# Kernel tuning notes

Hardware: AMD Instinct MI355X
Metric: run time of the kernel (lower is better)

Reference implementation:

```python
import jax, jax.numpy as jnp
import numpy as np

TOP_K_FREQ = 16


def setup_inputs() -> dict:
    key = jax.random.key(0)
    x = jax.random.normal(key, (64, 4096, 128), dtype=jnp.float32)
    return {"x": x}


def reference(x):
    B, L, C = x.shape
    freq = jnp.fft.rfft(x, axis=1)              # [B, F, C] complex, F = L//2 + 1
    F = freq.shape[1]
    k = min(TOP_K_FREQ, F)
    mag = jnp.abs(freq)                          # [B, F, C]
    # top-k over frequency axis, vectorized across (B, C)
    mag_bcf = jnp.transpose(mag, (0, 2, 1))      # [B, C, F]
    _, idx = jax.lax.top_k(mag_bcf, k)           # idx: [B, C, k]
    b_ix = jnp.arange(B)[:, None, None]
    c_ix = jnp.arange(C)[None, :, None]
    mask_bcf = jnp.zeros((B, C, F), dtype=x.dtype).at[b_ix, c_ix, idx].set(1.0)
    mask = jnp.transpose(mask_bcf, (0, 2, 1))    # [B, F, C]
    freq_filtered = freq * mask
    out = jnp.fft.irfft(freq_filtered, n=L, axis=1)  # [B, L, C]
    return out.astype(x.dtype)
```

## Files before the change

kernel.cpp:

```cpp
#include <hip/hip_runtime.h>


#define SWZ(i) ((i) ^ (((i) >> 4) & 15))

__device__ __forceinline__ int drev16(int x) {
  return ((x & 15) << 8) | (x & 0xF0) | ((x >> 8) & 15);
}

__device__ __forceinline__ float2 cmulf(float2 a, float c, float s) {
  return make_float2(a.x * c - a.y * s, a.x * s + a.y * c);
}

__device__ __forceinline__ void bfly4(float2& a0, float2& a1, float2& a2, float2& a3) {
  float ar = a0.x + a2.x, ai = a0.y + a2.y;
  float br = a0.x - a2.x, bi = a0.y - a2.y;
  float cr = a1.x + a3.x, ci = a1.y + a3.y;
  float dr = a1.x - a3.x, di = a1.y - a3.y;
  a0 = make_float2(ar + cr, ai + ci);
  a1 = make_float2(br + di, bi - dr);
  a2 = make_float2(ar - cr, ai - ci);
  a3 = make_float2(br - di, bi + dr);
}

__device__ __forceinline__ void dft16(float2* v) {
  const float C16[10] = {1.f, 0.9238795325112867f, 0.7071067811865476f, 0.3826834323650898f, 0.f,
                         -0.3826834323650898f, -0.7071067811865476f, -0.9238795325112867f, -1.f,
                         -0.9238795325112867f};
  const float S16[10] = {0.f, -0.3826834323650898f, -0.7071067811865476f, -0.9238795325112867f, -1.f,
                         -0.9238795325112867f, -0.7071067811865476f, -0.3826834323650898f, 0.f,
                         0.3826834323650898f};
  #pragma unroll
  for (int j2 = 0; j2 < 4; j2++) {
    bfly4(v[j2], v[j2 + 4], v[j2 + 8], v[j2 + 12]);
    if (j2 > 0) {
      v[j2 + 4]  = cmulf(v[j2 + 4],  C16[j2],     S16[j2]);
      v[j2 + 8]  = cmulf(v[j2 + 8],  C16[2 * j2], S16[2 * j2]);
      v[j2 + 12] = cmulf(v[j2 + 12], C16[3 * j2], S16[3 * j2]);
    }
  }
  #pragma unroll
  for (int r2 = 0; r2 < 4; r2++) bfly4(v[4 * r2], v[4 * r2 + 1], v[4 * r2 + 2], v[4 * r2 + 3]);
}

template <int STRIDE, int M>
__device__ __forceinline__ void fft_pass(float2* Zl, int base, int j) {
  const int kRev4[16] = {0, 4, 8, 12, 1, 5, 9, 13, 2, 6, 10, 14, 3, 7, 11, 15};
  float2 v[16];
  #pragma unroll
  for (int p = 0; p < 16; p++) v[p] = Zl[SWZ(base + j + STRIDE * p)];
  dft16(v);
  #pragma unroll
  for (int r = 0; r < 16; r++) {
    float2 u = v[kRev4[r]];
    if (M > 0 && r > 0) {
      int a = (j * r) & (M - 1);
      if (a > M / 2) a -= M;
      float ang = (float)a * (-6.2831853071795864769f / (float)M);
      float s, c;
      __sincosf(ang, &s, &c);
      u = cmulf(u, c, s);
    }
    Zl[SWZ(base + j + STRIDE * r)] = u;
  }
}


__global__ __launch_bounds__(256) void transpose_LC(
    const float4* __restrict__ X4, float4* __restrict__ T4) {
  __shared__ float tile[32 * 132];
  const int t = threadIdx.x;
  const int b = blockIdx.x >> 7;
  const int l0 = (blockIdx.x & 127) << 5;
  const float4* src = X4 + ((size_t)b * 4096 + l0) * 32;
  #pragma unroll
  for (int k = 0; k < 4; k++) {
    int idx = t + 256 * k;
    int l = idx >> 5, cf4 = idx & 31;
    float4 v = src[l * 32 + cf4];
    const float* a = (const float*)&v;
    #pragma unroll
    for (int j = 0; j < 4; j++) tile[l * 132 + 4 * cf4 + j] = a[j];
  }
  __syncthreads();
  float4* dst = T4 + (size_t)b * 128 * 1024 + (l0 >> 2);
  #pragma unroll
  for (int k = 0; k < 4; k++) {
    int idx = t + 256 * k;
    int c = idx >> 3, f = idx & 7;
    float4 w;
    float* o = (float*)&w;
    #pragma unroll
    for (int j = 0; j < 4; j++) o[j] = tile[(4 * f + j) * 132 + c];
    dst[(size_t)c * 1024 + f] = w;
  }
}


__global__ __launch_bounds__(512, 2) void fourier_fwd_topk(
    float4* __restrict__ T4) {
  __shared__ float2 Za[4096];
  __shared__ float2 Zb[4096];

  const int tid = threadIdx.x;
  const int b = blockIdx.x >> 5;
  const int q = blockIdx.x & 31;
  const size_t rowbase = ((size_t)b * 128 + 4 * q) * 1024;

  #pragma unroll
  for (int k = 0; k < 4; k++) {
    int idx = tid + 512 * k;
    int hf = idx >> 10, p = idx & 1023;
    float4 v0 = T4[rowbase + (size_t)(2 * hf + 0) * 1024 + p];
    float4 v1 = T4[rowbase + (size_t)(2 * hf + 1) * 1024 + p];
    const float* a0 = (const float*)&v0;
    const float* a1 = (const float*)&v1;
    float2* Zt = hf ? Zb : Za;
    #pragma unroll
    for (int j = 0; j < 4; j++) Zt[SWZ(4 * p + j)] = make_float2(a0[j], a1[j]);
  }
  __syncthreads();

  const int h = tid >> 8;
  const int lt = tid & 255;
  float2* Zl = h ? Zb : Za;

  fft_pass<256, 4096>(Zl, 0, lt);
  __syncthreads();
  fft_pass<16, 256>(Zl, (lt >> 4) << 8, lt & 15);
  __syncthreads();
  fft_pass<1, 0>(Zl, lt << 4, 0);
  __syncthreads();

  const int wv = lt >> 6;
  const int lane = lt & 63;

  if (wv < 2) {
    const int ch = wv;
    int rF = 0; float rA = 0.f, rB = 0.f;
    float m2[32];
    #pragma unroll
    for (int k = 0; k < 32; k++) {
      int f = lane + (k << 6);
      float2 P = Zl[SWZ(drev16(f))];
      float2 Q = Zl[SWZ(drev16((4096 - f) & 4095))];
      float xr = ch ? (P.y + Q.y) : (P.x + Q.x);
      float xi = ch ? (Q.x - P.x) : (P.y - Q.y);
      m2[k] = xr * xr + xi * xi;
    }
    float m2x = -1.f;
    if (lane == 0) {
      float2 P = Zl[SWZ(8)];
      float t = ch ? P.y : P.x;
      m2x = 4.f * t * t;
    }
    for (int r = 0; r < 16; r++) {
      float bv = -1e30f; int bf = 0;
      #pragma unroll
      for (int k = 0; k < 32; k++) {
        int f = lane + (k << 6);
        if (m2[k] > bv) { bv = m2[k]; bf = f; }
      }
      if (m2x > bv) { bv = m2x; bf = 2048; }
      #pragma unroll
      for (int off = 32; off; off >>= 1) {
        float ov = __shfl_down(bv, off);
        int   of = __shfl_down(bf, off);
        if (ov > bv || (ov == bv && of < bf)) { bv = ov; bf = of; }
      }
      bf = __shfl(bf, 0);
      if (lane == r) {
        rF = bf;
        float2 P = Zl[SWZ(drev16(bf))];
        float2 Q = Zl[SWZ(drev16((4096 - bf) & 4095))];
        rA = ch ? 0.5f * (P.y + Q.y) : 0.5f * (P.x + Q.x);
        rB = ch ? 0.5f * (Q.x - P.x) : 0.5f * (P.y - Q.y);
      }
      if (bf == 2048) {
        if (lane == 0) m2x = -2.f;
      } else if ((bf & 63) == lane) {
        int kk = bf >> 6;
        #pragma unroll
        for (int k = 0; k < 32; k++) if (k == kk) m2[k] = -2.f;
      }
    }

    if (lane < 16) {
      const float inv = 2.44140625e-4f;
      float w = (rF == 0 || rF == 2048) ? inv : 2.f * inv;
      int c = 4 * q + 2 * h + wv;
      T4[((size_t)b * 128 + c) * 1024 + lane] =
          make_float4((float)rF, w * rA, -w * rB, 0.f);
    }
  }
}


__global__ __launch_bounds__(256) void synth_kernel(
    const float4* __restrict__ T4, float* __restrict__ out) {
  __shared__ float fS[16 * 132];
  __shared__ float aS[16 * 132];
  __shared__ float bS[16 * 132];
  const int t = threadIdx.x;
  const int b = blockIdx.x >> 7;
  const int l0 = (blockIdx.x & 127) << 5;

  #pragma unroll
  for (int i = 0; i < 8; i++) {
    int idx = t + 256 * i;
    int c = idx >> 4, s = idx & 15;
    float4 v = T4[((size_t)b * 128 + c) * 1024 + s];
    fS[s * 132 + c] = v.x;
    aS[s * 132 + c] = v.y;
    bS[s * 132 + c] = v.z;
  }
  __syncthreads();

  const int c = t & 127;
  const int seg = t >> 7;
  float fk[16], ak[16], bk[16];
  #pragma unroll
  for (int k = 0; k < 16; k++) {
    fk[k] = fS[k * 132 + c];
    ak[k] = aS[k * 132 + c];
    bk[k] = bS[k * 132 + c];
  }

  float* op = out + ((size_t)b * 4096 + l0) * 128 + c;
  for (int p = 0; p < 16; p++) {
    float lf = (float)(l0 + 2 * p + seg);
    float acc = 0.f;
    #pragma unroll
    for (int k = 0; k < 16; k++) {
      float x = fk[k] * lf * 2.44140625e-4f;
      x = x - floorf(x);
      float sn = __builtin_amdgcn_sinf(x);
      float cs = __builtin_amdgcn_cosf(x);
      acc = fmaf(ak[k], cs, fmaf(bk[k], sn, acc));
    }
    op[(size_t)(2 * p + seg) * 128] = acc;
  }
}

extern "C" void kernel_launch(void* const* d_in, const int* in_sizes, int n_in,
                              void* d_out, int out_size, void* d_ws, size_t ws_size,
                              hipStream_t stream) {
  (void)in_sizes; (void)n_in; (void)ws_size; (void)out_size;
  const float4* x = (const float4*)d_in[0];
  float* out = (float*)d_out;
  float4* xT = (float4*)d_ws;

  transpose_LC<<<dim3(64 * 128), dim3(256), 0, stream>>>(x, xT);
  fourier_fwd_topk<<<dim3(64 * 32), dim3(512), 0, stream>>>(xT);
  synth_kernel<<<dim3(64 * 128), dim3(256), 0, stream>>>(xT, out);
}
```

Baseline: 612.6 us.

## Drop transpose kernel, read strided input directly; use rotation recurrence in synthesis

```diff
diff --git a/kernel.cpp b/kernel.cpp
--- a/kernel.cpp
+++ b/kernel.cpp
@@ -65,58 +65,23 @@
 }
 
 
-__global__ __launch_bounds__(256) void transpose_LC(
-    const float4* __restrict__ X4, float4* __restrict__ T4) {
-  __shared__ float tile[32 * 132];
-  const int t = threadIdx.x;
-  const int b = blockIdx.x >> 7;
-  const int l0 = (blockIdx.x & 127) << 5;
-  const float4* src = X4 + ((size_t)b * 4096 + l0) * 32;
-  #pragma unroll
-  for (int k = 0; k < 4; k++) {
-    int idx = t + 256 * k;
-    int l = idx >> 5, cf4 = idx & 31;
-    float4 v = src[l * 32 + cf4];
-    const float* a = (const float*)&v;
-    #pragma unroll
-    for (int j = 0; j < 4; j++) tile[l * 132 + 4 * cf4 + j] = a[j];
-  }
-  __syncthreads();
-  float4* dst = T4 + (size_t)b * 128 * 1024 + (l0 >> 2);
-  #pragma unroll
-  for (int k = 0; k < 4; k++) {
-    int idx = t + 256 * k;
-    int c = idx >> 3, f = idx & 7;
-    float4 w;
-    float* o = (float*)&w;
-    #pragma unroll
-    for (int j = 0; j < 4; j++) o[j] = tile[(4 * f + j) * 132 + c];
-    dst[(size_t)c * 1024 + f] = w;
-  }
-}
-
-
 __global__ __launch_bounds__(512, 2) void fourier_fwd_topk(
-    float4* __restrict__ T4) {
+    const float4* __restrict__ X4, float4* __restrict__ W4) {
   __shared__ float2 Za[4096];
   __shared__ float2 Zb[4096];
 
   const int tid = threadIdx.x;
-  const int b = blockIdx.x >> 5;
-  const int q = blockIdx.x & 31;
-  const size_t rowbase = ((size_t)b * 128 + 4 * q) * 1024;
-
-  #pragma unroll
-  for (int k = 0; k < 4; k++) {
-    int idx = tid + 512 * k;
-    int hf = idx >> 10, p = idx & 1023;
-    float4 v0 = T4[rowbase + (size_t)(2 * hf + 0) * 1024 + p];
-    float4 v1 = T4[rowbase + (size_t)(2 * hf + 1) * 1024 + p];
-    const float* a0 = (const float*)&v0;
-    const float* a1 = (const float*)&v1;
-    float2* Zt = hf ? Zb : Za;
-    #pragma unroll
-    for (int j = 0; j < 4; j++) Zt[SWZ(4 * p + j)] = make_float2(a0[j], a1[j]);
+  const int o = ((blockIdx.x & 7) << 8) + (blockIdx.x >> 3);
+  const int b = o >> 5;
+  const int q = o & 31;
+
+  const float4* src = X4 + (size_t)b * 4096 * 32 + q;
+  #pragma unroll
+  for (int k = 0; k < 8; k++) {
+    int l = tid + 512 * k;
+    float4 v = src[(size_t)l * 32];
+    Za[SWZ(l)] = make_float2(v.x, v.y);
+    Zb[SWZ(l)] = make_float2(v.z, v.w);
   }
   __syncthreads();
 
@@ -188,7 +153,7 @@
       const float inv = 2.44140625e-4f;
       float w = (rF == 0 || rF == 2048) ? inv : 2.f * inv;
       int c = 4 * q + 2 * h + wv;
-      T4[((size_t)b * 128 + c) * 1024 + lane] =
+      W4[((size_t)b * 128 + c) * 16 + lane] =
           make_float4((float)rF, w * rA, -w * rB, 0.f);
     }
   }
@@ -196,7 +161,7 @@
 
 
 __global__ __launch_bounds__(256) void synth_kernel(
-    const float4* __restrict__ T4, float* __restrict__ out) {
+    const float4* __restrict__ W4, float* __restrict__ out) {
   __shared__ float fS[16 * 132];
   __shared__ float aS[16 * 132];
   __shared__ float bS[16 * 132];
@@ -208,7 +173,7 @@
   for (int i = 0; i < 8; i++) {
     int idx = t + 256 * i;
     int c = idx >> 4, s = idx & 15;
-    float4 v = T4[((size_t)b * 128 + c) * 1024 + s];
+    float4 v = W4[((size_t)b * 128 + c) * 16 + s];
     fS[s * 132 + c] = v.x;
     aS[s * 132 + c] = v.y;
     bS[s * 132 + c] = v.z;
@@ -217,25 +182,32 @@
 
   const int c = t & 127;
   const int seg = t >> 7;
-  float fk[16], ak[16], bk[16];
+  float ak[16], bk[16], ck[16], sk[16], dc[16], ds[16];
+  const float lsf = (float)(l0 + seg);
   #pragma unroll
   for (int k = 0; k < 16; k++) {
-    fk[k] = fS[k * 132 + c];
+    float f = fS[k * 132 + c];
     ak[k] = aS[k * 132 + c];
     bk[k] = bS[k * 132 + c];
+    float x0 = f * lsf * 2.44140625e-4f;
+    x0 = x0 - floorf(x0);
+    ck[k] = __builtin_amdgcn_cosf(x0);
+    sk[k] = __builtin_amdgcn_sinf(x0);
+    float dx = f * 4.8828125e-4f;
+    dx = dx - floorf(dx);
+    dc[k] = __builtin_amdgcn_cosf(dx);
+    ds[k] = __builtin_amdgcn_sinf(dx);
   }
 
   float* op = out + ((size_t)b * 4096 + l0) * 128 + c;
   for (int p = 0; p < 16; p++) {
-    float lf = (float)(l0 + 2 * p + seg);
     float acc = 0.f;
     #pragma unroll
     for (int k = 0; k < 16; k++) {
-      float x = fk[k] * lf * 2.44140625e-4f;
-      x = x - floorf(x);
-      float sn = __builtin_amdgcn_sinf(x);
-      float cs = __builtin_amdgcn_cosf(x);
-      acc = fmaf(ak[k], cs, fmaf(bk[k], sn, acc));
+      acc = fmaf(ak[k], ck[k], fmaf(bk[k], sk[k], acc));
+      float nc = fmaf(ck[k], dc[k], -sk[k] * ds[k]);
+      float ns = fmaf(sk[k], dc[k],  ck[k] * ds[k]);
+      ck[k] = nc; sk[k] = ns;
     }
     op[(size_t)(2 * p + seg) * 128] = acc;
   }
@@ -247,9 +219,8 @@
   (void)in_sizes; (void)n_in; (void)ws_size; (void)out_size;
   const float4* x = (const float4*)d_in[0];
   float* out = (float*)d_out;
-  float4* xT = (float4*)d_ws;
-
-  transpose_LC<<<dim3(64 * 128), dim3(256), 0, stream>>>(x, xT);
-  fourier_fwd_topk<<<dim3(64 * 32), dim3(512), 0, stream>>>(xT);
-  synth_kernel<<<dim3(64 * 128), dim3(256), 0, stream>>>(xT, out);
-}
+  float4* W = (float4*)d_ws;
+
+  fourier_fwd_topk<<<dim3(64 * 32), dim3(512), 0, stream>>>(x, W);
+  synth_kernel<<<dim3(64 * 128), dim3(256), 0, stream>>>(W, out);
+}
```

New measurement: 565.2 us. 7.7% less time.
